# Kernel tuning notes

Measured on AMD Instinct MI355X. Metric: run time of the kernel, lower is better.

Reference implementation:

```python
import jax, jax.numpy as jnp
import numpy as np

N = 100000      # nodes
E = 400000      # edges
F_IN = 602      # Reddit features
H = 256         # hidden
C = 42          # classes


def setup_inputs() -> dict:
    key = jax.random.key(0)
    ks = jax.random.split(key, 8)
    x = jax.random.normal(ks[0], (N, F_IN), dtype=jnp.float32)
    edge_index = jax.random.randint(ks[1], (2, E), 0, N, dtype=jnp.int32)
    s1 = 1.0 / np.sqrt(F_IN)
    s2 = 1.0 / np.sqrt(H)
    return {
        "x": x,
        "edge_index": edge_index,
        # layer 1 (SAGEConv: lin_l on aggregated neighbors w/ bias, lin_r on root no bias)
        "Wl1": jax.random.uniform(ks[2], (F_IN, H), jnp.float32, -s1, s1),
        "bl1": jnp.zeros((H,), jnp.float32),
        "Wr1": jax.random.uniform(ks[3], (F_IN, H), jnp.float32, -s1, s1),
        # layer 2
        "Wl2": jax.random.uniform(ks[4], (H, C), jnp.float32, -s2, s2),
        "bl2": jnp.zeros((C,), jnp.float32),
        "Wr2": jax.random.uniform(ks[5], (H, C), jnp.float32, -s2, s2),
    }


def _sage_conv(x, src, dst, Wl, bl, Wr, num_nodes):
    # gather source features along edges, mean-aggregate per destination node
    msgs = x[src]                                               # [E, F]
    summed = jax.ops.segment_sum(msgs, dst, num_segments=num_nodes)  # [N, F]
    cnt = jax.ops.segment_sum(jnp.ones((src.shape[0], 1), x.dtype), dst,
                              num_segments=num_nodes)           # [N, 1]
    mean = summed / jnp.maximum(cnt, 1.0)                       # isolated nodes -> 0
    return mean @ Wl + bl + x @ Wr


def reference(x, edge_index, Wl1, bl1, Wr1, Wl2, bl2, Wr2):
    src, dst = edge_index[0], edge_index[1]
    n = x.shape[0]
    h = jax.nn.relu(_sage_conv(x, src, dst, Wl1, bl1, Wr1, n))
    # dropout is identity in eval mode
    out = _sage_conv(h, src, dst, Wl2, bl2, Wr2, n)
    return jax.nn.log_softmax(out, axis=1)
```

## Files before the change

### kernel.cpp

```cpp
#include <hip/hip_runtime.h>
#include <stdint.h>

#define NN 100000
#define NE 400000
#define FIN 602
#define HID 256
#define NC 42
#define NB_SCAN 98

typedef __attribute__((ext_vector_type(8))) short bf16x8;
typedef __attribute__((ext_vector_type(4))) float f32x4;
typedef __attribute__((ext_vector_type(2))) float f32x2;
typedef __attribute__((ext_vector_type(4))) short s16x4;

static __device__ __forceinline__ short f2bf(float f) {
  union { float f; uint32_t u; } v; v.f = f;
  uint32_t r = (v.u + 0x7fffu + ((v.u >> 16) & 1u)) >> 16;
  return (short)(uint16_t)r;
}
static __device__ __forceinline__ float bf2f(short s) {
  union { uint32_t u; float f; } v; v.u = ((uint32_t)(uint16_t)s) << 16;
  return v.f;
}
static __device__ __forceinline__ uint32_t cvtpk(float a, float b) {
  uint32_t r;
  asm("v_cvt_pk_bf16_f32 %0, %1, %2" : "=v"(r) : "v"(a), "v"(b));
  return r;
}
static __device__ __forceinline__ bf16x8 pack8q(f32x4 a, f32x4 b) {
  union { bf16x8 v; uint32_t u[4]; } r;
  r.u[0] = cvtpk(a[0], a[1]);
  r.u[1] = cvtpk(a[2], a[3]);
  r.u[2] = cvtpk(b[0], b[1]);
  r.u[3] = cvtpk(b[2], b[3]);
  return r.v;
}
static __device__ __forceinline__ void gload_lds4(const float* g, float* lds) {
  __builtin_amdgcn_global_load_lds((const __attribute__((address_space(1))) void*)g,
                                   (__attribute__((address_space(3))) void*)lds, 4, 0, 0);
}

__global__ __launch_bounds__(256) void k_count(const int* __restrict__ dst, int* __restrict__ cnt) {
  int t = blockIdx.x * 256 + threadIdx.x;
  if (t < NE) atomicAdd(&cnt[dst[t]], 1);
}

__global__ __launch_bounds__(1024) void k_scan_local(const int* __restrict__ cnt, int* __restrict__ rowptr,
                                                     int* __restrict__ bsum) {
  __shared__ int sm[1024];
  int tid = threadIdx.x, t = blockIdx.x * 1024 + tid;
  int v = (t < NN) ? cnt[t] : 0;
  sm[tid] = v;
  __syncthreads();
  for (int off = 1; off < 1024; off <<= 1) {
    int y = (tid >= off) ? sm[tid - off] : 0;
    __syncthreads();
    sm[tid] += y;
    __syncthreads();
  }
  if (t < NN) rowptr[t] = sm[tid] - v;
  if (tid == 1023) bsum[blockIdx.x] = sm[tid];
}
__global__ __launch_bounds__(128) void k_scan_bsum(int* __restrict__ bsum) {
  __shared__ int sm[128];
  int tid = threadIdx.x;
  int v = (tid < NB_SCAN) ? bsum[tid] : 0;
  sm[tid] = v;
  __syncthreads();
  for (int off = 1; off < 128; off <<= 1) {
    int y = (tid >= off) ? sm[tid - off] : 0;
    __syncthreads();
    sm[tid] += y;
    __syncthreads();
  }
  if (tid < NB_SCAN) bsum[tid] = sm[tid] - v;
}
__global__ __launch_bounds__(1024) void k_scan_add(int* __restrict__ rowptr, const int* __restrict__ bsum) {
  int t = blockIdx.x * 1024 + threadIdx.x;
  if (t < NN) rowptr[t] += bsum[t >> 10];
  if (t == 0) rowptr[NN] = NE;
}

__global__ __launch_bounds__(256) void k_sort(const int* __restrict__ src, const int* __restrict__ dst,
                                              const int* __restrict__ rowptr, int* __restrict__ epos,
                                              int* __restrict__ esorted) {
  int t = blockIdx.x * 256 + threadIdx.x;
  if (t >= NE) return;
  int d = dst[t];
  int p = atomicAdd(&epos[d], 1);
  esorted[rowptr[d] + p] = src[t];
}

__global__ __launch_bounds__(256) void k_prep_w1(const float* __restrict__ Wl, const float* __restrict__ Wr,
                                                 short* __restrict__ wf) {
  int idx = blockIdx.x * 256 + threadIdx.x;
  if (idx >= 32 * 19 * 512) return;
  int i = idx & 7, l = (idx >> 3) & 63, rest = idx >> 9;
  int ks = rest % 19, ct = rest / 19;
  int c = ct * 16 + (l & 15);
  int k = ks * 32 + ((l >> 4) << 3) + i;
  float v = 0.f;
  if (k < FIN) v = (c < HID) ? Wl[k * HID + c] : Wr[k * HID + (c - HID)];
  wf[idx] = f2bf(v);
}
__global__ __launch_bounds__(256) void k_prep_w2(const float* __restrict__ Wl, const float* __restrict__ Wr,
                                                 short* __restrict__ wf) {
  int idx = blockIdx.x * 256 + threadIdx.x;
  if (idx >= 6 * 8 * 512) return;
  int i = idx & 7, l = (idx >> 3) & 63, rest = idx >> 9;
  int ks = rest & 7, ct = rest >> 3;
  int c = ct * 16 + (l & 15);
  int k = ks * 32 + ((l >> 4) << 3) + i;
  float v = 0.f;
  if (c < NC) v = Wl[k * NC + c];
  else if (c < 2 * NC) v = Wr[k * NC + (c - NC)];
  wf[idx] = f2bf(v);
}

__global__ __launch_bounds__(256) void k_gemm_l1(const float* __restrict__ x, const short* __restrict__ wf,
                                                 short* __restrict__ t1, short* __restrict__ t2) {
  __shared__ float xs[2][64 * 32];
  const int lane = threadIdx.x & 63;
  const int w = threadIdx.x >> 6;
  const int lr = lane & 15, lg = lane >> 4;
  const int row0 = blockIdx.x * 64;

  f32x4 acc[4][8];
#pragma unroll
  for (int a = 0; a < 4; ++a)
#pragma unroll
    for (int b = 0; b < 8; ++b)
      acc[a][b] = (f32x4){0.f, 0.f, 0.f, 0.f};

  const short* wbL = wf + (size_t)(w * 4) * 19 * 512 + lane * 8;
  const short* wbR = wf + (size_t)(16 + w * 4) * 19 * 512 + lane * 8;

  const int s_rhalf = lane >> 5;
  const int s_pq = (lane & 31) >> 2;
  const int s_pe = lane & 3;

#define STAGE(KS, BUF)                                                                   \
  {                                                                                      \
    _Pragma("unroll")                                                                    \
    for (int q = 0; q < 8; ++q) {                                                        \
      int r = w * 16 + 2 * q + s_rhalf;                                                  \
      int rs = row0 + r; rs = rs < NN ? rs : NN - 1;                                     \
      int ld = ((s_pq ^ (r & 7)) << 2) | s_pe;                                           \
      int k = (KS) * 32 + ld;                                                            \
      k = k < FIN ? k : 0;                                                               \
      gload_lds4(x + (size_t)rs * FIN + k, &xs[BUF][(w * 16 + 2 * q) * 32]);             \
    }                                                                                    \
  }

  STAGE(0, 0);
  __syncthreads();

  for (int ks = 0; ks < 19; ++ks) {
    const int cur = ks & 1;
    if (ks < 18) STAGE(ks + 1, cur ^ 1);
    bf16x8 bbL[4], bbR[4];
#pragma unroll
    for (int c = 0; c < 4; ++c) bbL[c] = *(const bf16x8*)(wbL + (size_t)(c * 19 + ks) * 512);
#pragma unroll
    for (int c = 0; c < 4; ++c) bbR[c] = *(const bf16x8*)(wbR + (size_t)(c * 19 + ks) * 512);
    bf16x8 af[4];
#pragma unroll
    for (int t = 0; t < 4; ++t) {
      const char* rowp = (const char*)&xs[cur][(t * 16 + lr) * 32];
      f32x4 v0 = *(const f32x4*)(rowp + (((lg * 2 + 0) ^ (lr & 7)) << 4));
      f32x4 v1 = *(const f32x4*)(rowp + (((lg * 2 + 1) ^ (lr & 7)) << 4));
      af[t] = pack8q(v0, v1);
    }
#pragma unroll
    for (int c = 0; c < 4; ++c)
#pragma unroll
      for (int t = 0; t < 4; ++t) {
        acc[t][c]     = __builtin_amdgcn_mfma_f32_16x16x32_bf16(af[t], bbL[c], acc[t][c], 0, 0, 0);
        acc[t][4 + c] = __builtin_amdgcn_mfma_f32_16x16x32_bf16(af[t], bbR[c], acc[t][4 + c], 0, 0, 0);
      }
    __syncthreads();
  }
#undef STAGE

#pragma unroll
  for (int t = 0; t < 4; ++t)
#pragma unroll
    for (int c = 0; c < 8; ++c)
#pragma unroll
      for (int j = 0; j < 4; ++j) {
        int row = row0 + t * 16 + lg * 4 + j;
        if (row < NN) {
          int col = w * 64 + (c & 3) * 16 + lr;
          short* dstb = (c < 4) ? t1 : t2;
          dstb[(size_t)row * HID + col] = f2bf(acc[t][c][j]);
        }
      }
}

__global__ __launch_bounds__(256) void k_gather1(const short* __restrict__ t1, short* __restrict__ t2h,
                                                 const int* __restrict__ rowptr, const int* __restrict__ esorted,
                                                 const float* __restrict__ bl) {
  int t = blockIdx.x * 256 + threadIdx.x;
  int n = t >> 6, lane = t & 63;
  if (n >= NN) return;
  s16x4 tv = *(const s16x4*)(t2h + (size_t)n * HID + lane * 4);
  int beg = rowptr[n], end = rowptr[n + 1];
  float a0 = 0.f, a1 = 0.f, a2 = 0.f, a3 = 0.f;
  for (int j = beg; j < end; ++j) {
    int s = esorted[j];
    s16x4 v = *(const s16x4*)(t1 + (size_t)s * HID + lane * 4);
    a0 += bf2f(v[0]); a1 += bf2f(v[1]); a2 += bf2f(v[2]); a3 += bf2f(v[3]);
  }
  int deg = end - beg;
  float inv = 1.0f / (float)(deg > 1 ? deg : 1);
  f32x4 b = *(const f32x4*)(bl + lane * 4);
  s16x4 o;
  float v0 = a0 * inv + b[0] + bf2f(tv[0]);
  float v1 = a1 * inv + b[1] + bf2f(tv[1]);
  float v2 = a2 * inv + b[2] + bf2f(tv[2]);
  float v3 = a3 * inv + b[3] + bf2f(tv[3]);
  o[0] = f2bf(v0 > 0.f ? v0 : 0.f);
  o[1] = f2bf(v1 > 0.f ? v1 : 0.f);
  o[2] = f2bf(v2 > 0.f ? v2 : 0.f);
  o[3] = f2bf(v3 > 0.f ? v3 : 0.f);
  *(s16x4*)(t2h + (size_t)n * HID + lane * 4) = o;
}

__global__ __launch_bounds__(256) void k_gemm2(const short* __restrict__ h, const short* __restrict__ wf,
                                               float* __restrict__ u) {
  const int lane = threadIdx.x & 63;
  const int w = threadIdx.x >> 6;
  const int lr = lane & 15, lg = lane >> 4;
  const int row0 = blockIdx.x * 128 + w * 32;

  f32x4 acc[2][6];
#pragma unroll
  for (int a = 0; a < 2; ++a)
#pragma unroll
    for (int b = 0; b < 6; ++b)
      acc[a][b] = (f32x4){0.f, 0.f, 0.f, 0.f};

  const int r0 = row0 + lr, r1 = row0 + 16 + lr;
#pragma unroll
  for (int ks = 0; ks < 8; ++ks) {
    bf16x8 a0, a1;
#pragma unroll
    for (int i = 0; i < 8; ++i) { a0[i] = 0; a1[i] = 0; }
    if (r0 < NN) a0 = *(const bf16x8*)(h + (size_t)r0 * HID + ks * 32 + lg * 8);
    if (r1 < NN) a1 = *(const bf16x8*)(h + (size_t)r1 * HID + ks * 32 + lg * 8);
    bf16x8 bfrag[6];
#pragma unroll
    for (int ct = 0; ct < 6; ++ct)
      bfrag[ct] = *(const bf16x8*)(wf + (size_t)((ct * 8 + ks) * 64 + lane) * 8);
#pragma unroll
    for (int ct = 0; ct < 6; ++ct) {
      acc[0][ct] = __builtin_amdgcn_mfma_f32_16x16x32_bf16(a0, bfrag[ct], acc[0][ct], 0, 0, 0);
      acc[1][ct] = __builtin_amdgcn_mfma_f32_16x16x32_bf16(a1, bfrag[ct], acc[1][ct], 0, 0, 0);
    }
  }
#pragma unroll
  for (int rt = 0; rt < 2; ++rt)
#pragma unroll
    for (int ct = 0; ct < 6; ++ct)
#pragma unroll
      for (int j = 0; j < 4; ++j) {
        int row = row0 + rt * 16 + lg * 4 + j;
        int col = ct * 16 + lr;
        if (row < NN) u[(size_t)row * 96 + col] = acc[rt][ct][j];
      }
}

__global__ __launch_bounds__(256) void k_final(const float* __restrict__ u, const int* __restrict__ rowptr,
                                               const int* __restrict__ esorted, const float* __restrict__ bl,
                                               float* __restrict__ out) {
  int t = blockIdx.x * 256 + threadIdx.x;
  int n = t >> 6, c = t & 63;
  if (n >= NN) return;
  int beg = rowptr[n], end = rowptr[n + 1];
  float a = 0.f;
  if (c < NC) {
    for (int j = beg; j < end; ++j) {
      int s = esorted[j];
      a += u[(size_t)s * 96 + c];
    }
  }
  int deg = end - beg;
  float inv = 1.0f / (float)(deg > 1 ? deg : 1);
  float v = (c < NC) ? (a * inv + bl[c] + u[(size_t)n * 96 + NC + c]) : -1e30f;
  float m = v;
#pragma unroll
  for (int off = 32; off > 0; off >>= 1) m = fmaxf(m, __shfl_xor(m, off));
  float e = (c < NC) ? __expf(v - m) : 0.f;
#pragma unroll
  for (int off = 32; off > 0; off >>= 1) e += __shfl_xor(e, off);
  float lse = __logf(e);
  if (c < NC) out[(size_t)n * NC + c] = v - m - lse;
}

extern "C" void kernel_launch(void* const* d_in, const int* in_sizes, int n_in,
                              void* d_out, int out_size, void* d_ws, size_t ws_size,
                              hipStream_t stream) {
  const float* x   = (const float*)d_in[0];
  const int* eidx  = (const int*)d_in[1];
  const float* Wl1 = (const float*)d_in[2];
  const float* bl1 = (const float*)d_in[3];
  const float* Wr1 = (const float*)d_in[4];
  const float* Wl2 = (const float*)d_in[5];
  const float* bl2 = (const float*)d_in[6];
  const float* Wr2 = (const float*)d_in[7];
  float* out = (float*)d_out;
  const int* src = eidx;
  const int* dstp = eidx + NE;

  char* ws = (char*)d_ws;
  int*   cnt     = (int*)(ws + 0);
  int*   rowptr  = (int*)(ws + 524288);
  int*   epos    = (int*)(ws + 1048576);
  int*   bsum    = (int*)(ws + 1462272);
  short* wf1     = (short*)(ws + 1572864);
  short* wf2     = (short*)(ws + 2359296);
  int*   esorted = (int*)(ws + 2621440);
  short* t1      = (short*)(ws + 4300800);
  short* t2h     = (short*)(ws + 55500800);
  float* u       = (float*)(ws + 4300800);

  hipMemsetAsync(cnt, 0, (size_t)NN * sizeof(int), stream);
  hipMemsetAsync(epos, 0, (size_t)NN * sizeof(int), stream);
  k_prep_w1<<<(32 * 19 * 512 + 255) / 256, 256, 0, stream>>>(Wl1, Wr1, wf1);
  k_prep_w2<<<(6 * 8 * 512 + 255) / 256, 256, 0, stream>>>(Wl2, Wr2, wf2);
  k_count<<<(NE + 255) / 256, 256, 0, stream>>>(dstp, cnt);
  k_scan_local<<<NB_SCAN, 1024, 0, stream>>>(cnt, rowptr, bsum);
  k_scan_bsum<<<1, 128, 0, stream>>>(bsum);
  k_scan_add<<<NB_SCAN, 1024, 0, stream>>>(rowptr, bsum);
  k_sort<<<(NE + 255) / 256, 256, 0, stream>>>(src, dstp, rowptr, epos, esorted);
  k_gemm_l1<<<(NN + 63) / 64, 256, 0, stream>>>(x, wf1, t1, t2h);
  k_gather1<<<(NN * 64) / 256, 256, 0, stream>>>(t1, t2h, rowptr, esorted, bl1);
  k_gemm2<<<(NN + 127) / 128, 256, 0, stream>>>(t2h, wf2, u);
  k_final<<<(NN * 64) / 256, 256, 0, stream>>>(u, rowptr, esorted, bl2, out);
}
```

Before: 708.2 us.

## Split layer-1 GEMM over output halves with 64-wide K tiles; unroll gathers

New measurement: 641.2 us. -9.5%, faster.

```diff
diff --git a/kernel.cpp b/kernel.cpp
--- a/kernel.cpp
+++ b/kernel.cpp
@@ -94,9 +94,9 @@
 __global__ __launch_bounds__(256) void k_prep_w1(const float* __restrict__ Wl, const float* __restrict__ Wr,
                                                  short* __restrict__ wf) {
   int idx = blockIdx.x * 256 + threadIdx.x;
-  if (idx >= 32 * 19 * 512) return;
+  if (idx >= 32 * 20 * 512) return;
   int i = idx & 7, l = (idx >> 3) & 63, rest = idx >> 9;
-  int ks = rest % 19, ct = rest / 19;
+  int ks = rest % 20, ct = rest / 20;
   int c = ct * 16 + (l & 15);
   int k = ks * 32 + ((l >> 4) << 3) + i;
   float v = 0.f;
@@ -119,79 +119,82 @@
 
 __global__ __launch_bounds__(256) void k_gemm_l1(const float* __restrict__ x, const short* __restrict__ wf,
                                                  short* __restrict__ t1, short* __restrict__ t2) {
-  __shared__ float xs[2][64 * 32];
+  __shared__ float xs[2][64 * 64];
   const int lane = threadIdx.x & 63;
   const int w = threadIdx.x >> 6;
   const int lr = lane & 15, lg = lane >> 4;
+  const int wc = w & 1, wr = w >> 1;
   const int row0 = blockIdx.x * 64;
-
-  f32x4 acc[4][8];
-#pragma unroll
-  for (int a = 0; a < 4; ++a)
+  const int bn = blockIdx.y;
+
+  f32x4 acc[2][8];
+#pragma unroll
+  for (int a = 0; a < 2; ++a)
 #pragma unroll
     for (int b = 0; b < 8; ++b)
       acc[a][b] = (f32x4){0.f, 0.f, 0.f, 0.f};
 
-  const short* wbL = wf + (size_t)(w * 4) * 19 * 512 + lane * 8;
-  const short* wbR = wf + (size_t)(16 + w * 4) * 19 * 512 + lane * 8;
-
-  const int s_rhalf = lane >> 5;
-  const int s_pq = (lane & 31) >> 2;
-  const int s_pe = lane & 3;
-
-#define STAGE(KS, BUF)                                                                   \
-  {                                                                                      \
-    _Pragma("unroll")                                                                    \
-    for (int q = 0; q < 8; ++q) {                                                        \
-      int r = w * 16 + 2 * q + s_rhalf;                                                  \
-      int rs = row0 + r; rs = rs < NN ? rs : NN - 1;                                     \
-      int ld = ((s_pq ^ (r & 7)) << 2) | s_pe;                                           \
-      int k = (KS) * 32 + ld;                                                            \
-      k = k < FIN ? k : 0;                                                               \
-      gload_lds4(x + (size_t)rs * FIN + k, &xs[BUF][(w * 16 + 2 * q) * 32]);             \
-    }                                                                                    \
+  const short* wb = wf + (size_t)(bn * 16 + wc * 8) * 20 * 512 + lane * 8;
+
+  const int s_pq = lane >> 2, s_pe = lane & 3;
+
+#define STAGE(KS, BUF)                                                             \
+  {                                                                                \
+    _Pragma("unroll")                                                              \
+    for (int q = 0; q < 16; ++q) {                                                 \
+      int r = w * 16 + q;                                                          \
+      int rs = row0 + r; rs = rs < NN ? rs : NN - 1;                               \
+      int ld = ((s_pq ^ (r & 15)) << 2) | s_pe;                                    \
+      int k = (KS) * 64 + ld; k = k < FIN ? k : 0;                                 \
+      gload_lds4(x + (size_t)rs * FIN + k, &xs[BUF][r * 64]);                      \
+    }                                                                              \
   }
 
   STAGE(0, 0);
   __syncthreads();
 
-  for (int ks = 0; ks < 19; ++ks) {
+  for (int ks = 0; ks < 10; ++ks) {
     const int cur = ks & 1;
-    if (ks < 18) STAGE(ks + 1, cur ^ 1);
-    bf16x8 bbL[4], bbR[4];
-#pragma unroll
-    for (int c = 0; c < 4; ++c) bbL[c] = *(const bf16x8*)(wbL + (size_t)(c * 19 + ks) * 512);
-#pragma unroll
-    for (int c = 0; c < 4; ++c) bbR[c] = *(const bf16x8*)(wbR + (size_t)(c * 19 + ks) * 512);
-    bf16x8 af[4];
-#pragma unroll
-    for (int t = 0; t < 4; ++t) {
-      const char* rowp = (const char*)&xs[cur][(t * 16 + lr) * 32];
-      f32x4 v0 = *(const f32x4*)(rowp + (((lg * 2 + 0) ^ (lr & 7)) << 4));
-      f32x4 v1 = *(const f32x4*)(rowp + (((lg * 2 + 1) ^ (lr & 7)) << 4));
-      af[t] = pack8q(v0, v1);
+    bf16x8 bb0[8], bb1[8];
+#pragma unroll
+    for (int c = 0; c < 8; ++c) bb0[c] = *(const bf16x8*)(wb + (size_t)(c * 20 + ks * 2) * 512);
+#pragma unroll
+    for (int c = 0; c < 8; ++c) bb1[c] = *(const bf16x8*)(wb + (size_t)(c * 20 + ks * 2 + 1) * 512);
+    if (ks < 9) STAGE(ks + 1, cur ^ 1);
+#pragma unroll
+    for (int s = 0; s < 2; ++s) {
+      bf16x8 af[2];
+#pragma unroll
+      for (int t = 0; t < 2; ++t) {
+        int row = wr * 32 + t * 16 + lr;
+        const char* rowp = (const char*)&xs[cur][row * 64];
+        int lq0 = s * 8 + lg * 2;
+        f32x4 v0 = *(const f32x4*)(rowp + ((((lq0 + 0) ^ lr) & 15) << 4));
+        f32x4 v1 = *(const f32x4*)(rowp + ((((lq0 + 1) ^ lr) & 15) << 4));
+        af[t] = pack8q(v0, v1);
+      }
+#pragma unroll
+      for (int c = 0; c < 8; ++c) {
+        bf16x8 bbv = s ? bb1[c] : bb0[c];
+#pragma unroll
+        for (int t = 0; t < 2; ++t)
+          acc[t][c] = __builtin_amdgcn_mfma_f32_16x16x32_bf16(af[t], bbv, acc[t][c], 0, 0, 0);
+      }
     }
-#pragma unroll
-    for (int c = 0; c < 4; ++c)
-#pragma unroll
-      for (int t = 0; t < 4; ++t) {
-        acc[t][c]     = __builtin_amdgcn_mfma_f32_16x16x32_bf16(af[t], bbL[c], acc[t][c], 0, 0, 0);
-        acc[t][4 + c] = __builtin_amdgcn_mfma_f32_16x16x32_bf16(af[t], bbR[c], acc[t][4 + c], 0, 0, 0);
-      }
     __syncthreads();
   }
 #undef STAGE
 
-#pragma unroll
-  for (int t = 0; t < 4; ++t)
+  short* dstb = (bn == 0) ? t1 : t2;
+#pragma unroll
+  for (int t = 0; t < 2; ++t)
 #pragma unroll
     for (int c = 0; c < 8; ++c)
 #pragma unroll
       for (int j = 0; j < 4; ++j) {
-        int row = row0 + t * 16 + lg * 4 + j;
+        int row = row0 + wr * 32 + t * 16 + lg * 4 + j;
         if (row < NN) {
-          int col = w * 64 + (c & 3) * 16 + lr;
-          short* dstb = (c < 4) ? t1 : t2;
+          int col = (wc * 8 + c) * 16 + lr;
           dstb[(size_t)row * HID + col] = f2bf(acc[t][c][j]);
         }
       }
@@ -206,7 +209,19 @@
   s16x4 tv = *(const s16x4*)(t2h + (size_t)n * HID + lane * 4);
   int beg = rowptr[n], end = rowptr[n + 1];
   float a0 = 0.f, a1 = 0.f, a2 = 0.f, a3 = 0.f;
-  for (int j = beg; j < end; ++j) {
+  int j = beg;
+  for (; j + 4 <= end; j += 4) {
+    int s0 = esorted[j], s1 = esorted[j + 1], s2 = esorted[j + 2], s3 = esorted[j + 3];
+    s16x4 v0 = *(const s16x4*)(t1 + (size_t)s0 * HID + lane * 4);
+    s16x4 v1 = *(const s16x4*)(t1 + (size_t)s1 * HID + lane * 4);
+    s16x4 v2 = *(const s16x4*)(t1 + (size_t)s2 * HID + lane * 4);
+    s16x4 v3 = *(const s16x4*)(t1 + (size_t)s3 * HID + lane * 4);
+    a0 += bf2f(v0[0]) + bf2f(v1[0]) + bf2f(v2[0]) + bf2f(v3[0]);
+    a1 += bf2f(v0[1]) + bf2f(v1[1]) + bf2f(v2[1]) + bf2f(v3[1]);
+    a2 += bf2f(v0[2]) + bf2f(v1[2]) + bf2f(v2[2]) + bf2f(v3[2]);
+    a3 += bf2f(v0[3]) + bf2f(v1[3]) + bf2f(v2[3]) + bf2f(v3[3]);
+  }
+  for (; j < end; ++j) {
     int s = esorted[j];
     s16x4 v = *(const s16x4*)(t1 + (size_t)s * HID + lane * 4);
     a0 += bf2f(v[0]); a1 += bf2f(v[1]); a2 += bf2f(v[2]); a3 += bf2f(v[3]);
@@ -279,10 +294,16 @@
   int beg = rowptr[n], end = rowptr[n + 1];
   float a = 0.f;
   if (c < NC) {
-    for (int j = beg; j < end; ++j) {
-      int s = esorted[j];
-      a += u[(size_t)s * 96 + c];
+    int j = beg;
+    for (; j + 4 <= end; j += 4) {
+      int s0 = esorted[j], s1 = esorted[j + 1], s2 = esorted[j + 2], s3 = esorted[j + 3];
+      float u0 = u[(size_t)s0 * 96 + c];
+      float u1 = u[(size_t)s1 * 96 + c];
+      float u2 = u[(size_t)s2 * 96 + c];
+      float u3 = u[(size_t)s3 * 96 + c];
+      a += (u0 + u1) + (u2 + u3);
     }
+    for (; j < end; ++j) a += u[(size_t)esorted[j] * 96 + c];
   }
   int deg = end - beg;
   float inv = 1.0f / (float)(deg > 1 ? deg : 1);
@@ -326,14 +347,15 @@
 
   hipMemsetAsync(cnt, 0, (size_t)NN * sizeof(int), stream);
   hipMemsetAsync(epos, 0, (size_t)NN * sizeof(int), stream);
-  k_prep_w1<<<(32 * 19 * 512 + 255) / 256, 256, 0, stream>>>(Wl1, Wr1, wf1);
+  k_prep_w1<<<(32 * 20 * 512 + 255) / 256, 256, 0, stream>>>(Wl1, Wr1, wf1);
   k_prep_w2<<<(6 * 8 * 512 + 255) / 256, 256, 0, stream>>>(Wl2, Wr2, wf2);
   k_count<<<(NE + 255) / 256, 256, 0, stream>>>(dstp, cnt);
   k_scan_local<<<NB_SCAN, 1024, 0, stream>>>(cnt, rowptr, bsum);
   k_scan_bsum<<<1, 128, 0, stream>>>(bsum);
   k_scan_add<<<NB_SCAN, 1024, 0, stream>>>(rowptr, bsum);
   k_sort<<<(NE + 255) / 256, 256, 0, stream>>>(src, dstp, rowptr, epos, esorted);
-  k_gemm_l1<<<(NN + 63) / 64, 256, 0, stream>>>(x, wf1, t1, t2h);
+  dim3 g1((NN + 63) / 64, 2);
+  k_gemm_l1<<<g1, 256, 0, stream>>>(x, wf1, t1, t2h);
   k_gather1<<<(NN * 64) / 256, 256, 0, stream>>>(t1, t2h, rowptr, esorted, bl1);
   k_gemm2<<<(NN + 127) / 128, 256, 0, stream>>>(t2h, wf2, u);
   k_final<<<(NN * 64) / 256, 256, 0, stream>>>(u, rowptr, esorted, bl2, out);
```
